# Performance work log

Measured on AMD Instinct MI355X. Metric: run time of the kernel, lower is better.

The kernel has to match this reference:

```python
import jax, jax.numpy as jnp
import numpy as np

N = 4_194_304   # batch
DIM = 2         # dim
K = 5           # n_potentials
EPS = 1.0       # epsilon
S_INIT = 0.1    # S_diagonal_init


def setup_inputs() -> dict:
    key = jax.random.key(0)
    k1, k2, k3, k4 = jax.random.split(key, 4)
    x = jax.random.normal(k1, (N, DIM), dtype=jnp.float32)
    r = jax.random.normal(k2, (K, DIM), dtype=jnp.float32)
    log_S = jnp.log(S_INIT * jnp.ones((K, DIM), dtype=jnp.float32))
    log_alpha = jnp.log(jnp.ones(K, dtype=jnp.float32) / K)
    # pre-drawn randomness for the mixture sample (one categorical + one normal per row)
    gumbel = jax.random.gumbel(k3, (N, K), dtype=jnp.float32)
    noise = jax.random.normal(k4, (N, DIM), dtype=jnp.float32)
    return {"x": x, "r": r, "log_S": log_S, "log_alpha": log_alpha,
            "gumbel": gumbel, "noise": noise}


def reference(x, r, log_S, log_alpha, gumbel, noise):
    # Fused equivalent of LightSBplus.forward: per-row diagonal-Gaussian
    S = jnp.exp(log_S)                                   # [K, D]
    logits = ((x * x) @ S.T + 2.0 * (x @ r.T)) / (2.0 * EPS) + log_alpha  # [N, K]
    idx = jnp.argmax(logits + gumbel, axis=-1)           # categorical sample, [N]
    Sk = S[idx]                                          # [N, D]
    rk = r[idx]                                          # [N, D]
    mean = rk + Sk * x                                   # r_k + S_k * x
    return mean + jnp.sqrt(EPS * Sk) * noise
```

## Files before the change

### kernel.cpp

```cpp
#include <hip/hip_runtime.h>
#include <math.h>

#define KPOT 5
#define ROWS_PER_BLOCK 1024
#define GUMBEL_FLOATS (ROWS_PER_BLOCK * KPOT)

__global__ __launch_bounds__(256) void lightsb_kernel(
    const float* __restrict__ x,
    const float* __restrict__ r,
    const float* __restrict__ log_S,
    const float* __restrict__ log_alpha,
    const float* __restrict__ gumbel,
    const float* __restrict__ noise,
    float* __restrict__ out,
    int n_rows)
{
    __shared__ float gsh[GUMBEL_FLOATS];

    const int t = threadIdx.x;
    const long long blockRow0 = (long long)blockIdx.x * ROWS_PER_BLOCK;

    float S0[KPOT], S1[KPOT], r0[KPOT], r1[KPOT], la[KPOT], q0[KPOT], q1[KPOT];

    if (blockRow0 + ROWS_PER_BLOCK <= n_rows) {
        const float4* x4 = reinterpret_cast<const float4*>(x) + blockRow0 / 2;
        const float4* n4 = reinterpret_cast<const float4*>(noise) + blockRow0 / 2;
        float4 xa = x4[t];
        float4 xb = x4[256 + t];
        float4 na = n4[t];
        float4 nb = n4[256 + t];

        const float4* g4 = reinterpret_cast<const float4*>(gumbel) + blockRow0 * KPOT / 4;
        float4* gsh4 = reinterpret_cast<float4*>(gsh);
#pragma unroll
        for (int j = 0; j < 5; ++j)
            gsh4[j * 256 + t] = g4[j * 256 + t];

#pragma unroll
        for (int k = 0; k < KPOT; ++k) {
            float s0 = expf(log_S[2 * k + 0]);
            float s1 = expf(log_S[2 * k + 1]);
            S0[k] = s0;  S1[k] = s1;
            r0[k] = r[2 * k + 0];  r1[k] = r[2 * k + 1];
            la[k] = log_alpha[k];
            q0[k] = sqrtf(s0);  q1[k] = sqrtf(s1);
        }

        __syncthreads();

        float4* o4 = reinterpret_cast<float4*>(out) + blockRow0 / 2;

#pragma unroll
        for (int p = 0; p < 2; ++p) {
            const float4 xv = (p == 0) ? xa : xb;
            const float4 nv = (p == 0) ? na : nb;
            const int lr0 = p * 512 + 2 * t;
            const float* g0 = &gsh[lr0 * KPOT];
            float ov[4];

#pragma unroll
            for (int h = 0; h < 2; ++h) {
                const float xx0 = (h == 0) ? xv.x : xv.z;
                const float xx1 = (h == 0) ? xv.y : xv.w;
                const float nn0 = (h == 0) ? nv.x : nv.z;
                const float nn1 = (h == 0) ? nv.y : nv.w;
                const float* g = g0 + h * KPOT;

                const float u0 = 0.5f * xx0 * xx0;
                const float u1 = 0.5f * xx1 * xx1;

                float best = fmaf(S0[0], u0, fmaf(S1[0], u1,
                             fmaf(r0[0], xx0, fmaf(r1[0], xx1, la[0] + g[0]))));
                float bS0 = S0[0], bS1 = S1[0];
                float br0 = r0[0], br1 = r1[0];
                float bq0 = q0[0], bq1 = q1[0];
#pragma unroll
                for (int k = 1; k < KPOT; ++k) {
                    float s = fmaf(S0[k], u0, fmaf(S1[k], u1,
                              fmaf(r0[k], xx0, fmaf(r1[k], xx1, la[k] + g[k]))));
                    bool c = s > best;
                    best = c ? s : best;
                    bS0 = c ? S0[k] : bS0;
                    bS1 = c ? S1[k] : bS1;
                    br0 = c ? r0[k] : br0;
                    br1 = c ? r1[k] : br1;
                    bq0 = c ? q0[k] : bq0;
                    bq1 = c ? q1[k] : bq1;
                }
                ov[2 * h + 0] = fmaf(bS0, xx0, fmaf(bq0, nn0, br0));
                ov[2 * h + 1] = fmaf(bS1, xx1, fmaf(bq1, nn1, br1));
            }
            o4[p * 256 + t] = make_float4(ov[0], ov[1], ov[2], ov[3]);
        }
    } else {
#pragma unroll
        for (int k = 0; k < KPOT; ++k) {
            float s0 = expf(log_S[2 * k + 0]);
            float s1 = expf(log_S[2 * k + 1]);
            S0[k] = s0;  S1[k] = s1;
            r0[k] = r[2 * k + 0];  r1[k] = r[2 * k + 1];
            la[k] = log_alpha[k];
            q0[k] = sqrtf(s0);  q1[k] = sqrtf(s1);
        }
        for (long long row = blockRow0 + t; row < n_rows; row += 256) {
            float x0 = x[row * 2 + 0];
            float x1 = x[row * 2 + 1];
            float u0 = 0.5f * x0 * x0;
            float u1 = 0.5f * x1 * x1;
            float best = fmaf(S0[0], u0, fmaf(S1[0], u1,
                         fmaf(r0[0], x0, fmaf(r1[0], x1, la[0] + gumbel[row * KPOT + 0]))));
            int bidx = 0;
#pragma unroll
            for (int k = 1; k < KPOT; ++k) {
                float s = fmaf(S0[k], u0, fmaf(S1[k], u1,
                          fmaf(r0[k], x0, fmaf(r1[k], x1, la[k] + gumbel[row * KPOT + k]))));
                if (s > best) { best = s; bidx = k; }
            }
            float n0 = noise[row * 2 + 0];
            float n1 = noise[row * 2 + 1];
            out[row * 2 + 0] = fmaf(S0[bidx], x0, fmaf(q0[bidx], n0, r0[bidx]));
            out[row * 2 + 1] = fmaf(S1[bidx], x1, fmaf(q1[bidx], n1, r1[bidx]));
        }
    }
}

extern "C" void kernel_launch(void* const* d_in, const int* in_sizes, int n_in,
                              void* d_out, int out_size, void* d_ws, size_t ws_size,
                              hipStream_t stream) {
    const float* x         = (const float*)d_in[0];
    const float* r         = (const float*)d_in[1];
    const float* log_S     = (const float*)d_in[2];
    const float* log_alpha = (const float*)d_in[3];
    const float* gumbel    = (const float*)d_in[4];
    const float* noise     = (const float*)d_in[5];
    float* out = (float*)d_out;

    const int n_rows = in_sizes[0] / 2;
    const int grid = (n_rows + ROWS_PER_BLOCK - 1) / ROWS_PER_BLOCK;

    lightsb_kernel<<<grid, 256, 0, stream>>>(x, r, log_S, log_alpha,
                                             gumbel, noise, out, n_rows);
}
```

Baseline: 188.7 us.

## Use persistent grid with register prefetch and per-wave double-buffered gumbel staging

Launches a fixed grid of 1024 blocks that loop over 1024-row tiles, prefetching the next tile's gumbel, x and noise into registers while computing the current tile. Each wavefront stages only its own slice of gumbel in a double-buffered LDS region, so the block-wide __syncthreads is removed. The intent is to overlap memory loads with compute and cut launch/block scheduling overhead in this bandwidth-bound kernel. In exchange it uses more registers and LDS per block and gives less occupancy-driven latency hiding, since the grid is fixed.

```diff
diff --git a/kernel.cpp b/kernel.cpp
--- a/kernel.cpp
+++ b/kernel.cpp
@@ -2,10 +2,10 @@
 #include <math.h>
 
 #define KPOT 5
-#define ROWS_PER_BLOCK 1024
-#define GUMBEL_FLOATS (ROWS_PER_BLOCK * KPOT)
+#define ROWS_PER_TILE 1024
+#define GRID_BLOCKS 1024
 
-__global__ __launch_bounds__(256) void lightsb_kernel(
+__global__ __launch_bounds__(256, 4) void lightsb_kernel(
     const float* __restrict__ x,
     const float* __restrict__ r,
     const float* __restrict__ log_S,
@@ -15,69 +15,88 @@
     float* __restrict__ out,
     int n_rows)
 {
-    __shared__ float gsh[GUMBEL_FLOATS];
+    __shared__ float4 gsh[2 * 4 * 320];
 
     const int t = threadIdx.x;
-    const long long blockRow0 = (long long)blockIdx.x * ROWS_PER_BLOCK;
+    const int w = t >> 6;
+    const int L = t & 63;
+
+    const long long nTiles = n_rows / ROWS_PER_TILE;
+
+    long long tile = blockIdx.x;
+    float4 gv0[5], xv0[2], nv0[2];
+    if (tile < nTiles) {
+        const float4* g4 = reinterpret_cast<const float4*>(gumbel) + tile * 1280 + w * 320;
+        const float4* x4 = reinterpret_cast<const float4*>(x)      + tile * 512  + w * 128;
+        const float4* n4 = reinterpret_cast<const float4*>(noise)  + tile * 512  + w * 128;
+#pragma unroll
+        for (int j = 0; j < 5; ++j) gv0[j] = g4[j * 64 + L];
+        xv0[0] = x4[L];      xv0[1] = x4[64 + L];
+        nv0[0] = n4[L];      nv0[1] = n4[64 + L];
+    }
 
     float S0[KPOT], S1[KPOT], r0[KPOT], r1[KPOT], la[KPOT], q0[KPOT], q1[KPOT];
+#pragma unroll
+    for (int k = 0; k < KPOT; ++k) {
+        float s0 = expf(log_S[2 * k + 0]);
+        float s1 = expf(log_S[2 * k + 1]);
+        S0[k] = s0;  S1[k] = s1;
+        r0[k] = r[2 * k + 0];  r1[k] = r[2 * k + 1];
+        la[k] = log_alpha[k];
+        q0[k] = sqrtf(s0);  q1[k] = sqrtf(s1);
+    }
 
-    if (blockRow0 + ROWS_PER_BLOCK <= n_rows) {
-        const float4* x4 = reinterpret_cast<const float4*>(x) + blockRow0 / 2;
-        const float4* n4 = reinterpret_cast<const float4*>(noise) + blockRow0 / 2;
-        float4 xa = x4[t];
-        float4 xb = x4[256 + t];
-        float4 na = n4[t];
-        float4 nb = n4[256 + t];
+    int buf = 0;
+    if (tile < nTiles) {
+        float4* dst = gsh + w * 320;
+#pragma unroll
+        for (int j = 0; j < 5; ++j) dst[j * 64 + L] = gv0[j];
+    }
 
-        const float4* g4 = reinterpret_cast<const float4*>(gumbel) + blockRow0 * KPOT / 4;
-        float4* gsh4 = reinterpret_cast<float4*>(gsh);
+    while (tile < nTiles) {
+        const long long ntile = tile + GRID_BLOCKS;
+        const bool more = (ntile < nTiles);
+
+        float4 gv1[5], xv1[2], nv1[2];
+        if (more) {
+            const float4* g4 = reinterpret_cast<const float4*>(gumbel) + ntile * 1280 + w * 320;
 #pragma unroll
-        for (int j = 0; j < 5; ++j)
-            gsh4[j * 256 + t] = g4[j * 256 + t];
+            for (int j = 0; j < 5; ++j) gv1[j] = g4[j * 64 + L];
+            const float4* x4 = reinterpret_cast<const float4*>(x)     + ntile * 512 + w * 128;
+            const float4* n4 = reinterpret_cast<const float4*>(noise) + ntile * 512 + w * 128;
+            xv1[0] = x4[L];      xv1[1] = x4[64 + L];
+            nv1[0] = n4[L];      nv1[1] = n4[64 + L];
+        }
+
+        const float* gbase = reinterpret_cast<const float*>(gsh + buf * 1280 + w * 320);
+        float4* o4 = reinterpret_cast<float4*>(out) + tile * 512 + w * 128;
 
 #pragma unroll
-        for (int k = 0; k < KPOT; ++k) {
-            float s0 = expf(log_S[2 * k + 0]);
-            float s1 = expf(log_S[2 * k + 1]);
-            S0[k] = s0;  S1[k] = s1;
-            r0[k] = r[2 * k + 0];  r1[k] = r[2 * k + 1];
-            la[k] = log_alpha[k];
-            q0[k] = sqrtf(s0);  q1[k] = sqrtf(s1);
-        }
-
-        __syncthreads();
-
-        float4* o4 = reinterpret_cast<float4*>(out) + blockRow0 / 2;
-
+        for (int h = 0; h < 2; ++h) {
+            const float4 xv = xv0[h];
+            const float4 nv = nv0[h];
+            const float* g = gbase + h * 640 + 10 * L;
+            float ov[4];
 #pragma unroll
-        for (int p = 0; p < 2; ++p) {
-            const float4 xv = (p == 0) ? xa : xb;
-            const float4 nv = (p == 0) ? na : nb;
-            const int lr0 = p * 512 + 2 * t;
-            const float* g0 = &gsh[lr0 * KPOT];
-            float ov[4];
-
-#pragma unroll
-            for (int h = 0; h < 2; ++h) {
-                const float xx0 = (h == 0) ? xv.x : xv.z;
-                const float xx1 = (h == 0) ? xv.y : xv.w;
-                const float nn0 = (h == 0) ? nv.x : nv.z;
-                const float nn1 = (h == 0) ? nv.y : nv.w;
-                const float* g = g0 + h * KPOT;
+            for (int hh = 0; hh < 2; ++hh) {
+                const float xx0 = (hh == 0) ? xv.x : xv.z;
+                const float xx1 = (hh == 0) ? xv.y : xv.w;
+                const float nn0 = (hh == 0) ? nv.x : nv.z;
+                const float nn1 = (hh == 0) ? nv.y : nv.w;
+                const float* gg = g + hh * KPOT;
 
                 const float u0 = 0.5f * xx0 * xx0;
                 const float u1 = 0.5f * xx1 * xx1;
 
                 float best = fmaf(S0[0], u0, fmaf(S1[0], u1,
-                             fmaf(r0[0], xx0, fmaf(r1[0], xx1, la[0] + g[0]))));
+                             fmaf(r0[0], xx0, fmaf(r1[0], xx1, la[0] + gg[0]))));
                 float bS0 = S0[0], bS1 = S1[0];
                 float br0 = r0[0], br1 = r1[0];
                 float bq0 = q0[0], bq1 = q1[0];
 #pragma unroll
                 for (int k = 1; k < KPOT; ++k) {
                     float s = fmaf(S0[k], u0, fmaf(S1[k], u1,
-                              fmaf(r0[k], xx0, fmaf(r1[k], xx1, la[k] + g[k]))));
+                              fmaf(r0[k], xx0, fmaf(r1[k], xx1, la[k] + gg[k]))));
                     bool c = s > best;
                     best = c ? s : best;
                     bS0 = c ? S0[k] : bS0;
@@ -87,40 +106,43 @@
                     bq0 = c ? q0[k] : bq0;
                     bq1 = c ? q1[k] : bq1;
                 }
-                ov[2 * h + 0] = fmaf(bS0, xx0, fmaf(bq0, nn0, br0));
-                ov[2 * h + 1] = fmaf(bS1, xx1, fmaf(bq1, nn1, br1));
+                ov[2 * hh + 0] = fmaf(bS0, xx0, fmaf(bq0, nn0, br0));
+                ov[2 * hh + 1] = fmaf(bS1, xx1, fmaf(bq1, nn1, br1));
             }
-            o4[p * 256 + t] = make_float4(ov[0], ov[1], ov[2], ov[3]);
+            o4[h * 64 + L] = make_float4(ov[0], ov[1], ov[2], ov[3]);
         }
-    } else {
+
+        if (more) {
+            float4* dst = gsh + (buf ^ 1) * 1280 + w * 320;
 #pragma unroll
-        for (int k = 0; k < KPOT; ++k) {
-            float s0 = expf(log_S[2 * k + 0]);
-            float s1 = expf(log_S[2 * k + 1]);
-            S0[k] = s0;  S1[k] = s1;
-            r0[k] = r[2 * k + 0];  r1[k] = r[2 * k + 1];
-            la[k] = log_alpha[k];
-            q0[k] = sqrtf(s0);  q1[k] = sqrtf(s1);
+            for (int j = 0; j < 5; ++j) dst[j * 64 + L] = gv1[j];
+            xv0[0] = xv1[0];  xv0[1] = xv1[1];
+            nv0[0] = nv1[0];  nv0[1] = nv1[1];
         }
-        for (long long row = blockRow0 + t; row < n_rows; row += 256) {
-            float x0 = x[row * 2 + 0];
-            float x1 = x[row * 2 + 1];
-            float u0 = 0.5f * x0 * x0;
-            float u1 = 0.5f * x1 * x1;
-            float best = fmaf(S0[0], u0, fmaf(S1[0], u1,
-                         fmaf(r0[0], x0, fmaf(r1[0], x1, la[0] + gumbel[row * KPOT + 0]))));
-            int bidx = 0;
+        buf ^= 1;
+        tile = ntile;
+    }
+
+    for (long long row = nTiles * ROWS_PER_TILE + (long long)blockIdx.x * 256 + t;
+         row < n_rows;
+         row += (long long)GRID_BLOCKS * 256) {
+        float x0 = x[row * 2 + 0];
+        float x1 = x[row * 2 + 1];
+        float u0 = 0.5f * x0 * x0;
+        float u1 = 0.5f * x1 * x1;
+        float best = fmaf(S0[0], u0, fmaf(S1[0], u1,
+                     fmaf(r0[0], x0, fmaf(r1[0], x1, la[0] + gumbel[row * KPOT + 0]))));
+        int bidx = 0;
 #pragma unroll
-            for (int k = 1; k < KPOT; ++k) {
-                float s = fmaf(S0[k], u0, fmaf(S1[k], u1,
-                          fmaf(r0[k], x0, fmaf(r1[k], x1, la[k] + gumbel[row * KPOT + k]))));
-                if (s > best) { best = s; bidx = k; }
-            }
-            float n0 = noise[row * 2 + 0];
-            float n1 = noise[row * 2 + 1];
-            out[row * 2 + 0] = fmaf(S0[bidx], x0, fmaf(q0[bidx], n0, r0[bidx]));
-            out[row * 2 + 1] = fmaf(S1[bidx], x1, fmaf(q1[bidx], n1, r1[bidx]));
+        for (int k = 1; k < KPOT; ++k) {
+            float s = fmaf(S0[k], u0, fmaf(S1[k], u1,
+                      fmaf(r0[k], x0, fmaf(r1[k], x1, la[k] + gumbel[row * KPOT + k]))));
+            if (s > best) { best = s; bidx = k; }
         }
+        float n0 = noise[row * 2 + 0];
+        float n1 = noise[row * 2 + 1];
+        out[row * 2 + 0] = fmaf(S0[bidx], x0, fmaf(q0[bidx], n0, r0[bidx]));
+        out[row * 2 + 1] = fmaf(S1[bidx], x1, fmaf(q1[bidx], n1, r1[bidx]));
     }
 }
 
@@ -136,8 +158,7 @@
     float* out = (float*)d_out;
 
     const int n_rows = in_sizes[0] / 2;
-    const int grid = (n_rows + ROWS_PER_BLOCK - 1) / ROWS_PER_BLOCK;
 
-    lightsb_kernel<<<grid, 256, 0, stream>>>(x, r, log_S, log_alpha,
-                                             gumbel, noise, out, n_rows);
+    lightsb_kernel<<<GRID_BLOCKS, 256, 0, stream>>>(x, r, log_S, log_alpha,
+                                                    gumbel, noise, out, n_rows);
 }
```

New measurement: 204.0 us. 1.08x slower.

## Give each wavefront its own gumbel staging slice and drop block barrier

Applied to the files above, without the earlier changes.

Splits the 1024-row block into four wavefront-private 256-row slices, so each wave loads its own gumbel, x and noise data and stages gumbel through its own LDS region. This removes the block-wide __syncthreads between the shared-memory fill and the compute. It also adds a min-blocks hint to launch_bounds. The risk is relying on intra-wavefront LDS visibility without an explicit barrier.

```diff
diff --git a/kernel.cpp b/kernel.cpp
--- a/kernel.cpp
+++ b/kernel.cpp
@@ -3,9 +3,8 @@
 
 #define KPOT 5
 #define ROWS_PER_BLOCK 1024
-#define GUMBEL_FLOATS (ROWS_PER_BLOCK * KPOT)
 
-__global__ __launch_bounds__(256) void lightsb_kernel(
+__global__ __launch_bounds__(256, 4) void lightsb_kernel(
     const float* __restrict__ x,
     const float* __restrict__ r,
     const float* __restrict__ log_S,
@@ -15,26 +14,30 @@
     float* __restrict__ out,
     int n_rows)
 {
-    __shared__ float gsh[GUMBEL_FLOATS];
+    __shared__ float4 gsh[4 * 320];
 
     const int t = threadIdx.x;
+    const int w = t >> 6;
+    const int L = t & 63;
+
     const long long blockRow0 = (long long)blockIdx.x * ROWS_PER_BLOCK;
 
     float S0[KPOT], S1[KPOT], r0[KPOT], r1[KPOT], la[KPOT], q0[KPOT], q1[KPOT];
 
     if (blockRow0 + ROWS_PER_BLOCK <= n_rows) {
-        const float4* x4 = reinterpret_cast<const float4*>(x) + blockRow0 / 2;
-        const float4* n4 = reinterpret_cast<const float4*>(noise) + blockRow0 / 2;
-        float4 xa = x4[t];
-        float4 xb = x4[256 + t];
-        float4 na = n4[t];
-        float4 nb = n4[256 + t];
+        const float4* g4 = reinterpret_cast<const float4*>(gumbel)
+                           + blockRow0 * KPOT / 4 + w * 320;
+        float4 gv[5];
+#pragma unroll
+        for (int j = 0; j < 5; ++j) gv[j] = g4[j * 64 + L];
 
-        const float4* g4 = reinterpret_cast<const float4*>(gumbel) + blockRow0 * KPOT / 4;
-        float4* gsh4 = reinterpret_cast<float4*>(gsh);
-#pragma unroll
-        for (int j = 0; j < 5; ++j)
-            gsh4[j * 256 + t] = g4[j * 256 + t];
+        const float4* x4 = reinterpret_cast<const float4*>(x) + blockRow0 / 2 + w * 128;
+        float4 xa = x4[L];
+        float4 xb = x4[64 + L];
+
+        const float4* n4 = reinterpret_cast<const float4*>(noise) + blockRow0 / 2 + w * 128;
+        float4 na = n4[L];
+        float4 nb = n4[64 + L];
 
 #pragma unroll
         for (int k = 0; k < KPOT; ++k) {
@@ -46,25 +49,26 @@
             q0[k] = sqrtf(s0);  q1[k] = sqrtf(s1);
         }
 
-        __syncthreads();
+        float4* dst = gsh + w * 320;
+#pragma unroll
+        for (int j = 0; j < 5; ++j) dst[j * 64 + L] = gv[j];
 
-        float4* o4 = reinterpret_cast<float4*>(out) + blockRow0 / 2;
+        const float* gf = reinterpret_cast<const float*>(gsh + w * 320);
+        float4* o4 = reinterpret_cast<float4*>(out) + blockRow0 / 2 + w * 128;
 
 #pragma unroll
-        for (int p = 0; p < 2; ++p) {
-            const float4 xv = (p == 0) ? xa : xb;
-            const float4 nv = (p == 0) ? na : nb;
-            const int lr0 = p * 512 + 2 * t;
-            const float* g0 = &gsh[lr0 * KPOT];
+        for (int h = 0; h < 2; ++h) {
+            const float4 xv = (h == 0) ? xa : xb;
+            const float4 nv = (h == 0) ? na : nb;
+            const float* g0 = gf + h * 640 + 10 * L;
             float ov[4];
-
 #pragma unroll
-            for (int h = 0; h < 2; ++h) {
-                const float xx0 = (h == 0) ? xv.x : xv.z;
-                const float xx1 = (h == 0) ? xv.y : xv.w;
-                const float nn0 = (h == 0) ? nv.x : nv.z;
-                const float nn1 = (h == 0) ? nv.y : nv.w;
-                const float* g = g0 + h * KPOT;
+            for (int hh = 0; hh < 2; ++hh) {
+                const float xx0 = (hh == 0) ? xv.x : xv.z;
+                const float xx1 = (hh == 0) ? xv.y : xv.w;
+                const float nn0 = (hh == 0) ? nv.x : nv.z;
+                const float nn1 = (hh == 0) ? nv.y : nv.w;
+                const float* g = g0 + hh * KPOT;
 
                 const float u0 = 0.5f * xx0 * xx0;
                 const float u1 = 0.5f * xx1 * xx1;
@@ -87,10 +91,10 @@
                     bq0 = c ? q0[k] : bq0;
                     bq1 = c ? q1[k] : bq1;
                 }
-                ov[2 * h + 0] = fmaf(bS0, xx0, fmaf(bq0, nn0, br0));
-                ov[2 * h + 1] = fmaf(bS1, xx1, fmaf(bq1, nn1, br1));
+                ov[2 * hh + 0] = fmaf(bS0, xx0, fmaf(bq0, nn0, br0));
+                ov[2 * hh + 1] = fmaf(bS1, xx1, fmaf(bq1, nn1, br1));
             }
-            o4[p * 256 + t] = make_float4(ov[0], ov[1], ov[2], ov[3]);
+            o4[h * 64 + L] = make_float4(ov[0], ov[1], ov[2], ov[3]);
         }
     } else {
 #pragma unroll
```

After: 189.8 us. No clear change (+0.6%).
